# Kernel tuning notes

Hardware: AMD Instinct MI355X
Metric: run time of the kernel (lower is better)

Reference implementation:

```python
import jax, jax.numpy as jnp
import numpy as np

T, B, I, H, O = 512, 64, 512, 1024, 512
STDV = 1.0 / np.sqrt(H)


def setup_inputs() -> dict:
    key = jax.random.key(0)
    ks = jax.random.split(key, 12)
    u = lambda k, shape: jax.random.uniform(k, shape, jnp.float32, -STDV, STDV)
    return {
        "input": jax.random.normal(ks[0], (T, B, I), jnp.float32),
        "state": jnp.zeros((B, H), jnp.float32),
        "W_zh": u(ks[1], (H, H)), "W_zx": u(ks[2], (I, H)), "b_z": u(ks[3], (H,)),
        "W_rh": u(ks[4], (H, H)), "W_rx": u(ks[5], (I, H)), "b_r": u(ks[6], (H,)),
        "W_hh": u(ks[7], (H, H)), "W_hx": u(ks[8], (I, H)), "b_h": u(ks[9], (H,)),
        "W_out": u(ks[10], (O, H)), "b_out": u(ks[11], (O,)),
    }


def reference(input, state, W_zh, W_zx, b_z, W_rh, W_rx, b_r, W_hh, W_hx, b_h, W_out, b_out):
    # input: [T, B, I]; state: [B, H]
    def step(h, x):
        z = jax.nn.sigmoid(h @ W_zh + x @ W_zx + b_z)
        r = jax.nn.sigmoid(h @ W_rh + x @ W_rx + b_r)
        ht = jnp.tanh((h * r) @ W_hh + x @ W_hx + b_h)
        h = (1.0 - z) * h + z * ht
        y = h @ W_out.T + b_out  # Linear(hidim -> outdim)
        return h, y

    h_final, Y = jax.lax.scan(step, state, input)  # Y: [T, B, O]
    # torch.cat(Y, dim=0) -> [T*B, O]
    return Y.reshape(T * B, O), h_final
```

## Files before the change

### kernel.cpp

```cpp
#include <hip/hip_runtime.h>
#include <cstdint>


#define TT 512
#define BB 64
#define II 512
#define HH 1024
#define OO 512
#define NTHR 512

typedef float4 f4;
__device__ __forceinline__ f4 ld4(const float* p){ return *reinterpret_cast<const f4*>(p); }
__device__ __forceinline__ int swz(int k){ return k ^ (((k >> 4) & 7) << 2); }

__device__ __forceinline__ void ldc16(const float* p, f4* d){
  asm volatile(
    "global_load_dwordx4 %0,  %16, off sc0 sc1\n\t"
    "global_load_dwordx4 %1,  %16, off offset:256 sc0 sc1\n\t"
    "global_load_dwordx4 %2,  %16, off offset:512 sc0 sc1\n\t"
    "global_load_dwordx4 %3,  %16, off offset:768 sc0 sc1\n\t"
    "global_load_dwordx4 %4,  %16, off offset:1024 sc0 sc1\n\t"
    "global_load_dwordx4 %5,  %16, off offset:1280 sc0 sc1\n\t"
    "global_load_dwordx4 %6,  %16, off offset:1536 sc0 sc1\n\t"
    "global_load_dwordx4 %7,  %16, off offset:1792 sc0 sc1\n\t"
    "global_load_dwordx4 %8,  %16, off offset:2048 sc0 sc1\n\t"
    "global_load_dwordx4 %9,  %16, off offset:2304 sc0 sc1\n\t"
    "global_load_dwordx4 %10, %16, off offset:2560 sc0 sc1\n\t"
    "global_load_dwordx4 %11, %16, off offset:2816 sc0 sc1\n\t"
    "global_load_dwordx4 %12, %16, off offset:3072 sc0 sc1\n\t"
    "global_load_dwordx4 %13, %16, off offset:3328 sc0 sc1\n\t"
    "global_load_dwordx4 %14, %16, off offset:3584 sc0 sc1\n\t"
    "s_waitcnt vmcnt(1)\n\t"
    "global_load_dwordx4 %15, %16, off offset:3840 sc0 sc1\n\t"
    "s_waitcnt vmcnt(0)"
    : "=&v"(d[0]),"=&v"(d[1]),"=&v"(d[2]),"=&v"(d[3]),
      "=&v"(d[4]),"=&v"(d[5]),"=&v"(d[6]),"=&v"(d[7]),
      "=&v"(d[8]),"=&v"(d[9]),"=&v"(d[10]),"=&v"(d[11]),
      "=&v"(d[12]),"=&v"(d[13]),"=&v"(d[14]),"=&v"(d[15])
    : "v"(p) : "memory");
}
__device__ __forceinline__ float ldc1(const float* p){
  float v;
  asm volatile("global_load_dword %0, %1, off sc0 sc1\n\ts_waitcnt vmcnt(0)"
               : "=v"(v) : "v"(p) : "memory");
  return v;
}
__device__ __forceinline__ void stc1(float* p, float v){
  asm volatile("global_store_dword %0, %1, off sc0 sc1" :: "v"(p), "v"(v) : "memory");
}

__global__ void k_transpose_x(const float* __restrict__ x, float* __restrict__ xT){
  size_t total = (size_t)TT * II * BB;
  for (size_t n = (size_t)blockIdx.x * blockDim.x + threadIdx.x; n < total;
       n += (size_t)gridDim.x * blockDim.x){
    size_t t = n / ((size_t)II * BB);
    size_t rem = n % ((size_t)II * BB);
    size_t i = rem / BB, b = rem % BB;
    xT[n] = x[(t * BB + b) * II + i];
  }
}

__global__ void k_transpose_wx(const float* __restrict__ W, float* __restrict__ WT){
  size_t n = (size_t)blockIdx.x * blockDim.x + threadIdx.x;
  if (n >= (size_t)II * HH) return;
  size_t j = n / II, k = n % II;
  WT[n] = W[k * HH + j];
}

__global__ void k_transpose_h0(const float* __restrict__ st, float* __restrict__ h0){
  size_t n = (size_t)blockIdx.x * blockDim.x + threadIdx.x;
  if (n >= (size_t)HH * BB) return;
  size_t j = n / BB, b = n % BB;
  h0[n] = st[b * HH + j];
}

__global__ void k_init_bars(unsigned* bars){
  if (threadIdx.x < 512) bars[threadIdx.x] = 0;
}

__device__ __forceinline__ void g_arrive(unsigned* bars, int g, int jt, unsigned ep){
  asm volatile("s_waitcnt vmcnt(0)" ::: "memory");
  unsigned* leaf = bars + (g * 9 + (jt & 7)) * 16;
  unsigned old = __hip_atomic_fetch_add(leaf, 1u, __ATOMIC_RELAXED, __HIP_MEMORY_SCOPE_AGENT);
  if (old + 1u == ep * 16u)
    __hip_atomic_fetch_add(bars + (g * 9 + 8) * 16, 1u, __ATOMIC_RELAXED, __HIP_MEMORY_SCOPE_AGENT);
}
__device__ __forceinline__ void g_wait(unsigned* bars, int g, unsigned ep){
  unsigned* root = bars + (g * 9 + 8) * 16;
  while (__hip_atomic_load(root, __ATOMIC_RELAXED, __HIP_MEMORY_SCOPE_AGENT) < ep * 8u)
    __builtin_amdgcn_s_sleep(1);
}

#define WREDUCE(v) { v += __shfl_xor(v, 8); v += __shfl_xor(v, 16); v += __shfl_xor(v, 32); }

__global__ __launch_bounds__(NTHR, 2) void k_gru(
    const float* __restrict__ xT,
    const float* __restrict__ WxTr, const float* __restrict__ WxTz, const float* __restrict__ WxTh,
    float* __restrict__ h, float* __restrict__ s,
    const float* __restrict__ W_zh, const float* __restrict__ b_z,
    const float* __restrict__ W_rh, const float* __restrict__ b_r,
    const float* __restrict__ W_hh, const float* __restrict__ b_h,
    const float* __restrict__ W_out, const float* __restrict__ b_out,
    float* __restrict__ out, unsigned* __restrict__ bars)
{
  __shared__ float sW[3 * 8 * 1024];
  __shared__ float red[8 * 528];
  __shared__ float xpre[3][256];
  __shared__ float sZ[256];
  __shared__ float sBias[32];

  const int tid = threadIdx.x;
  const int bid = blockIdx.x;
  const int jt = bid & 127, bhalf = bid >> 7;
  const int j0 = jt * 8, o0 = jt * 4, bbase = bhalf * 32;

  #pragma unroll
  for (int kk2 = 0; kk2 < 2; ++kk2){
    const int k = tid * 2 + kk2;
    f4 vr  = ld4(W_rh + (size_t)k * HH + j0);
    f4 vr2 = ld4(W_rh + (size_t)k * HH + j0 + 4);
    f4 vz  = ld4(W_zh + (size_t)k * HH + j0);
    f4 vz2 = ld4(W_zh + (size_t)k * HH + j0 + 4);
    f4 vh  = ld4(W_hh + (size_t)k * HH + j0);
    f4 vh2 = ld4(W_hh + (size_t)k * HH + j0 + 4);
    const int kx = swz(k);
    float ar[8] = {vr.x,vr.y,vr.z,vr.w,vr2.x,vr2.y,vr2.z,vr2.w};
    float az[8] = {vz.x,vz.y,vz.z,vz.w,vz2.x,vz2.y,vz2.z,vz2.w};
    float ah[8] = {vh.x,vh.y,vh.z,vh.w,vh2.x,vh2.y,vh2.z,vh2.w};
    #pragma unroll
    for (int c = 0; c < 8; ++c){
      sW[0*8192 + c*1024 + kx] = ar[c];
      sW[1*8192 + c*1024 + kx] = az[c];
      sW[2*8192 + c*1024 + kx] = ah[c];
    }
  }
  if (tid < 8){
    sBias[tid]      = b_r[j0 + tid];
    sBias[8 + tid]  = b_z[j0 + tid];
    sBias[16 + tid] = b_h[j0 + tid];
    if (tid < 4) sBias[24 + tid] = b_out[o0 + tid];
  }

  const int bg = tid & 7, b0 = bbase + bg * 4;
  const int ksec = tid >> 3;
  const int wv = tid >> 6;
  const bool wr0 = ((tid & 56) == 0);
  const int kh0 = ksec * 16;
  const int kx0 = ksec * 8;
  __syncthreads();

  for (int t = -1; t < TT; ++t){
    f4 st4[16];
    if (t >= 0){
      float aR[8][4] = {};
      ldc16(h + kh0 * BB + b0, st4);
      #pragma unroll
      for (int i4 = 0; i4 < 4; ++i4){
        const int kxc = swz(kh0 + i4*4);
        #pragma unroll
        for (int c = 0; c < 8; ++c){
          f4 wf = *reinterpret_cast<const f4*>(&sW[0*8192 + c*1024 + kxc]);
          float wvv[4] = {wf.x, wf.y, wf.z, wf.w};
          #pragma unroll
          for (int kk = 0; kk < 4; ++kk){
            const f4 hv = st4[i4*4+kk];
            aR[c][0] = fmaf(wvv[kk], hv.x, aR[c][0]);
            aR[c][1] = fmaf(wvv[kk], hv.y, aR[c][1]);
            aR[c][2] = fmaf(wvv[kk], hv.z, aR[c][2]);
            aR[c][3] = fmaf(wvv[kk], hv.w, aR[c][3]);
          }
        }
      }
      #pragma unroll
      for (int c = 0; c < 8; ++c)
        #pragma unroll
        for (int bb = 0; bb < 4; ++bb) WREDUCE(aR[c][bb]);
      if (wr0)
        #pragma unroll
        for (int c = 0; c < 8; ++c)
          #pragma unroll
          for (int bb = 0; bb < 4; ++bb)
            red[wv*528 + c*32 + bg*4 + bb] = aR[c][bb];
      __syncthreads();
      if (tid < 256){
        float sum = 0.f;
        #pragma unroll
        for (int w = 0; w < 8; ++w) sum += red[w*528 + tid];
        const int c = tid >> 5, bl = tid & 31;
        const float v = sum + xpre[0][tid] + sBias[c];
        const float rr = 1.f / (1.f + expf(-v));
        const int jg = j0 + c, bgl = bbase + bl;
        stc1(&s[jg*BB + bgl], rr * ldc1(&h[jg*BB + bgl]));
      }
      __syncthreads();
      if (tid == 0) g_arrive(bars, bhalf, jt, 2*t + 1);

      float aZ[8][4] = {};
      float aY[4][4] = {};
      #pragma unroll
      for (int i4 = 0; i4 < 4; ++i4){
        const int kc = kh0 + i4*4;
        const int kxc = swz(kc);
        #pragma unroll
        for (int c = 0; c < 8; ++c){
          f4 wf = *reinterpret_cast<const f4*>(&sW[1*8192 + c*1024 + kxc]);
          float wvv[4] = {wf.x, wf.y, wf.z, wf.w};
          #pragma unroll
          for (int kk = 0; kk < 4; ++kk){
            const f4 hv = st4[i4*4+kk];
            aZ[c][0] = fmaf(wvv[kk], hv.x, aZ[c][0]);
            aZ[c][1] = fmaf(wvv[kk], hv.y, aZ[c][1]);
            aZ[c][2] = fmaf(wvv[kk], hv.z, aZ[c][2]);
            aZ[c][3] = fmaf(wvv[kk], hv.w, aZ[c][3]);
          }
        }
        #pragma unroll
        for (int oc = 0; oc < 4; ++oc){
          f4 wo = ld4(W_out + (size_t)(o0 + oc) * HH + kc);
          float wvv[4] = {wo.x, wo.y, wo.z, wo.w};
          #pragma unroll
          for (int kk = 0; kk < 4; ++kk){
            const f4 hv = st4[i4*4+kk];
            aY[oc][0] = fmaf(wvv[kk], hv.x, aY[oc][0]);
            aY[oc][1] = fmaf(wvv[kk], hv.y, aY[oc][1]);
            aY[oc][2] = fmaf(wvv[kk], hv.z, aY[oc][2]);
            aY[oc][3] = fmaf(wvv[kk], hv.w, aY[oc][3]);
          }
        }
      }
      #pragma unroll
      for (int c = 0; c < 8; ++c)
        #pragma unroll
        for (int bb = 0; bb < 4; ++bb) WREDUCE(aZ[c][bb]);
      #pragma unroll
      for (int oc = 0; oc < 4; ++oc)
        #pragma unroll
        for (int bb = 0; bb < 4; ++bb) WREDUCE(aY[oc][bb]);
      if (wr0){
        #pragma unroll
        for (int c = 0; c < 8; ++c)
          #pragma unroll
          for (int bb = 0; bb < 4; ++bb)
            red[wv*528 + c*32 + bg*4 + bb] = aZ[c][bb];
        #pragma unroll
        for (int oc = 0; oc < 4; ++oc)
          #pragma unroll
          for (int bb = 0; bb < 4; ++bb)
            red[wv*528 + 256 + oc*32 + bg*4 + bb] = aY[oc][bb];
      }
      __syncthreads();
      if (tid < 256){
        float sum = 0.f;
        #pragma unroll
        for (int w = 0; w < 8; ++w) sum += red[w*528 + tid];
        const int c = tid >> 5;
        sZ[tid] = 1.f / (1.f + expf(-(sum + xpre[1][tid] + sBias[8 + c])));
      } else if (tid < 384){
        const int idx = tid - 256;
        float sum = 0.f;
        #pragma unroll
        for (int w = 0; w < 8; ++w) sum += red[w*528 + tid];
        const int oc = idx >> 5, bl = idx & 31;
        if (t > 0)
          out[((size_t)(t-1)*BB + bbase + bl)*OO + o0 + oc] = sum + sBias[24 + oc];
      }
      if (tid == 0) g_wait(bars, bhalf, 2*t + 1);
      __syncthreads();

      float aH[8][4] = {};
      f4 sv16[16];
      ldc16(s + kh0 * BB + b0, sv16);
      #pragma unroll
      for (int i4 = 0; i4 < 4; ++i4){
        const int kxc = swz(kh0 + i4*4);
        #pragma unroll
        for (int c = 0; c < 8; ++c){
          f4 wf = *reinterpret_cast<const f4*>(&sW[2*8192 + c*1024 + kxc]);
          float wvv[4] = {wf.x, wf.y, wf.z, wf.w};
          #pragma unroll
          for (int kk = 0; kk < 4; ++kk){
            const f4 sv = sv16[i4*4+kk];
            aH[c][0] = fmaf(wvv[kk], sv.x, aH[c][0]);
            aH[c][1] = fmaf(wvv[kk], sv.y, aH[c][1]);
            aH[c][2] = fmaf(wvv[kk], sv.z, aH[c][2]);
            aH[c][3] = fmaf(wvv[kk], sv.w, aH[c][3]);
          }
        }
      }
      #pragma unroll
      for (int c = 0; c < 8; ++c)
        #pragma unroll
        for (int bb = 0; bb < 4; ++bb) WREDUCE(aH[c][bb]);
      if (wr0)
        #pragma unroll
        for (int c = 0; c < 8; ++c)
          #pragma unroll
          for (int bb = 0; bb < 4; ++bb)
            red[wv*528 + c*32 + bg*4 + bb] = aH[c][bb];
      __syncthreads();
      if (tid < 256){
        float sum = 0.f;
        #pragma unroll
        for (int w = 0; w < 8; ++w) sum += red[w*528 + tid];
        const int c = tid >> 5, bl = tid & 31;
        const int jg = j0 + c, bgl = bbase + bl;
        const float ht = tanhf(sum + xpre[2][tid] + sBias[16 + c]);
        const float z = sZ[tid];
        const float hold = ldc1(&h[jg*BB + bgl]);
        const float hnew = fmaf(z, ht - hold, hold);
        stc1(&h[jg*BB + bgl], hnew);
        if (t == TT - 1) out[(size_t)TT*BB*OO + (size_t)bgl*HH + jg] = hnew;
      }
      __syncthreads();
      if (tid == 0) g_arrive(bars, bhalf, jt, 2*t + 2);
    }

    if (t + 1 < TT){
      const int tc = t + 1;
      float aXr[8][4] = {}, aXz[8][4] = {}, aXh[8][4] = {};
      const float* xb = xT + (size_t)tc * II * BB + kx0 * BB + b0;
      #pragma unroll
      for (int i4 = 0; i4 < 2; ++i4){
        f4 xv4[4];
        #pragma unroll
        for (int kk = 0; kk < 4; ++kk) xv4[kk] = ld4(xb + (i4*4+kk) * BB);
        #pragma unroll
        for (int c = 0; c < 8; ++c){
          f4 wr_ = ld4(WxTr + (size_t)(j0 + c) * II + kx0 + i4*4);
          f4 wz_ = ld4(WxTz + (size_t)(j0 + c) * II + kx0 + i4*4);
          f4 wh_ = ld4(WxTh + (size_t)(j0 + c) * II + kx0 + i4*4);
          float wrv[4] = {wr_.x, wr_.y, wr_.z, wr_.w};
          float wzv[4] = {wz_.x, wz_.y, wz_.z, wz_.w};
          float whv[4] = {wh_.x, wh_.y, wh_.z, wh_.w};
          #pragma unroll
          for (int kk = 0; kk < 4; ++kk){
            const f4 xv = xv4[kk];
            aXr[c][0] = fmaf(wrv[kk], xv.x, aXr[c][0]);
            aXr[c][1] = fmaf(wrv[kk], xv.y, aXr[c][1]);
            aXr[c][2] = fmaf(wrv[kk], xv.z, aXr[c][2]);
            aXr[c][3] = fmaf(wrv[kk], xv.w, aXr[c][3]);
            aXz[c][0] = fmaf(wzv[kk], xv.x, aXz[c][0]);
            aXz[c][1] = fmaf(wzv[kk], xv.y, aXz[c][1]);
            aXz[c][2] = fmaf(wzv[kk], xv.z, aXz[c][2]);
            aXz[c][3] = fmaf(wzv[kk], xv.w, aXz[c][3]);
            aXh[c][0] = fmaf(whv[kk], xv.x, aXh[c][0]);
            aXh[c][1] = fmaf(whv[kk], xv.y, aXh[c][1]);
            aXh[c][2] = fmaf(whv[kk], xv.z, aXh[c][2]);
            aXh[c][3] = fmaf(whv[kk], xv.w, aXh[c][3]);
          }
        }
      }
      #pragma unroll
      for (int c = 0; c < 8; ++c)
        #pragma unroll
        for (int bb = 0; bb < 4; ++bb){ WREDUCE(aXr[c][bb]); WREDUCE(aXz[c][bb]); WREDUCE(aXh[c][bb]); }
      if (wr0)
        #pragma unroll
        for (int c = 0; c < 8; ++c)
          #pragma unroll
          for (int bb = 0; bb < 4; ++bb){
            red[wv*528 + c*32 + bg*4 + bb]       = aXr[c][bb];
            red[wv*528 + 256 + c*32 + bg*4 + bb] = aXz[c][bb];
          }
      __syncthreads();
      {
        float sum = 0.f;
        #pragma unroll
        for (int w = 0; w < 8; ++w) sum += red[w*528 + tid];
        if (tid < 256) xpre[0][tid] = sum;
        else           xpre[1][tid - 256] = sum;
      }
      __syncthreads();
      if (wr0)
        #pragma unroll
        for (int c = 0; c < 8; ++c)
          #pragma unroll
          for (int bb = 0; bb < 4; ++bb)
            red[wv*528 + c*32 + bg*4 + bb] = aXh[c][bb];
      __syncthreads();
      if (tid < 256){
        float sum = 0.f;
        #pragma unroll
        for (int w = 0; w < 8; ++w) sum += red[w*528 + tid];
        xpre[2][tid] = sum;
      }
      __syncthreads();
    }

    if (t >= 0){
      if (tid == 0) g_wait(bars, bhalf, 2*t + 2);
      __syncthreads();
    }
  }

  {
    float aY[4][4] = {};
    f4 hv16[16];
    ldc16(h + kh0 * BB + b0, hv16);
    #pragma unroll
    for (int i4 = 0; i4 < 4; ++i4){
      const int kc = kh0 + i4*4;
      #pragma unroll
      for (int oc = 0; oc < 4; ++oc){
        f4 wo = ld4(W_out + (size_t)(o0 + oc) * HH + kc);
        float wvv[4] = {wo.x, wo.y, wo.z, wo.w};
        #pragma unroll
        for (int kk = 0; kk < 4; ++kk){
          const f4 hv = hv16[i4*4+kk];
          aY[oc][0] = fmaf(wvv[kk], hv.x, aY[oc][0]);
          aY[oc][1] = fmaf(wvv[kk], hv.y, aY[oc][1]);
          aY[oc][2] = fmaf(wvv[kk], hv.z, aY[oc][2]);
          aY[oc][3] = fmaf(wvv[kk], hv.w, aY[oc][3]);
        }
      }
    }
    #pragma unroll
    for (int oc = 0; oc < 4; ++oc)
      #pragma unroll
      for (int bb = 0; bb < 4; ++bb) WREDUCE(aY[oc][bb]);
    if (wr0)
      #pragma unroll
      for (int oc = 0; oc < 4; ++oc)
        #pragma unroll
        for (int bb = 0; bb < 4; ++bb)
          red[wv*528 + oc*32 + bg*4 + bb] = aY[oc][bb];
    __syncthreads();
    if (tid < 128){
      float sum = 0.f;
      #pragma unroll
      for (int w = 0; w < 8; ++w) sum += red[w*528 + tid];
      const int oc = tid >> 5, bl = tid & 31;
      out[((size_t)(TT-1)*BB + bbase + bl)*OO + o0 + oc] = sum + sBias[24 + oc];
    }
  }
}

extern "C" void kernel_launch(void* const* d_in, const int* in_sizes, int n_in,
                              void* d_out, int out_size, void* d_ws, size_t ws_size,
                              hipStream_t stream) {
  const float* x     = (const float*)d_in[0];
  const float* st    = (const float*)d_in[1];
  const float* W_zh  = (const float*)d_in[2];
  const float* W_zx  = (const float*)d_in[3];
  const float* b_z   = (const float*)d_in[4];
  const float* W_rh  = (const float*)d_in[5];
  const float* W_rx  = (const float*)d_in[6];
  const float* b_r   = (const float*)d_in[7];
  const float* W_hh  = (const float*)d_in[8];
  const float* W_hx  = (const float*)d_in[9];
  const float* b_h   = (const float*)d_in[10];
  const float* W_out = (const float*)d_in[11];
  const float* b_out = (const float*)d_in[12];
  float* out = (float*)d_out;
  float* ws  = (float*)d_ws;

  const size_t xT_sz = (size_t)TT * II * BB;
  const size_t wx_sz = (size_t)II * HH;
  const size_t h_sz  = (size_t)HH * BB;
  const size_t need  = (xT_sz + 3*wx_sz + 2*h_sz) * sizeof(float) + 512*sizeof(unsigned);
  if (ws_size < need) return;

  float* xT   = ws;
  float* WxTr = xT + xT_sz;
  float* WxTz = WxTr + wx_sz;
  float* WxTh = WxTz + wx_sz;
  float* h    = WxTh + wx_sz;
  float* s    = h + h_sz;
  unsigned* bars = (unsigned*)(s + h_sz);

  k_transpose_x <<<8192, 256, 0, stream>>>(x, xT);
  k_transpose_wx<<<2048, 256, 0, stream>>>(W_rx, WxTr);
  k_transpose_wx<<<2048, 256, 0, stream>>>(W_zx, WxTz);
  k_transpose_wx<<<2048, 256, 0, stream>>>(W_hx, WxTh);
  k_transpose_h0<<< 256, 256, 0, stream>>>(st, h);
  k_init_bars   <<<   1, 512, 0, stream>>>(bars);

  k_gru<<<256, NTHR, 0, stream>>>(xT, WxTr, WxTz, WxTh, h, s,
                                  W_zh, b_z, W_rh, b_r, W_hh, b_h,
                                  W_out, b_out, out, bars);
}
```

Measured before the change: 12.98 ms.

## Read input directly in native layout, drop transpose kernel and LDS reduction

Removes the separate transpose of the full input sequence and has the GRU kernel read x in its original [T,B,I] layout. Each thread now handles one batch row and a contiguous 32-element k slice, so the x-projection partial sums are reduced entirely with intra-wavefront shuffles rather than through shared memory with three block barriers. This saves a large global read/write pass and several syncs per timestep. The cost is more weight-load traffic per thread, since each thread loads 32 k values of weights for a single batch element and gets less reuse than before.

```diff
diff --git a/kernel.cpp b/kernel.cpp
--- a/kernel.cpp
+++ b/kernel.cpp
@@ -49,17 +49,6 @@
   asm volatile("global_store_dword %0, %1, off sc0 sc1" :: "v"(p), "v"(v) : "memory");
 }
 
-__global__ void k_transpose_x(const float* __restrict__ x, float* __restrict__ xT){
-  size_t total = (size_t)TT * II * BB;
-  for (size_t n = (size_t)blockIdx.x * blockDim.x + threadIdx.x; n < total;
-       n += (size_t)gridDim.x * blockDim.x){
-    size_t t = n / ((size_t)II * BB);
-    size_t rem = n % ((size_t)II * BB);
-    size_t i = rem / BB, b = rem % BB;
-    xT[n] = x[(t * BB + b) * II + i];
-  }
-}
-
 __global__ void k_transpose_wx(const float* __restrict__ W, float* __restrict__ WT){
   size_t n = (size_t)blockIdx.x * blockDim.x + threadIdx.x;
   if (n >= (size_t)II * HH) return;
@@ -94,7 +83,7 @@
 #define WREDUCE(v) { v += __shfl_xor(v, 8); v += __shfl_xor(v, 16); v += __shfl_xor(v, 32); }
 
 __global__ __launch_bounds__(NTHR, 2) void k_gru(
-    const float* __restrict__ xT,
+    const float* __restrict__ x,
     const float* __restrict__ WxTr, const float* __restrict__ WxTz, const float* __restrict__ WxTh,
     float* __restrict__ h, float* __restrict__ s,
     const float* __restrict__ W_zh, const float* __restrict__ b_z,
@@ -146,7 +135,10 @@
   const int wv = tid >> 6;
   const bool wr0 = ((tid & 56) == 0);
   const int kh0 = ksec * 16;
-  const int kx0 = ksec * 8;
+
+  const int bC  = bbase + (tid >> 4);
+  const int ksC = tid & 15;
+  const int k0C = ksC * 32;
   __syncthreads();
 
   for (int t = -1; t < TT; ++t){
@@ -317,72 +309,48 @@
 
     if (t + 1 < TT){
       const int tc = t + 1;
-      float aXr[8][4] = {}, aXz[8][4] = {}, aXh[8][4] = {};
-      const float* xb = xT + (size_t)tc * II * BB + kx0 * BB + b0;
-      #pragma unroll
-      for (int i4 = 0; i4 < 2; ++i4){
-        f4 xv4[4];
-        #pragma unroll
-        for (int kk = 0; kk < 4; ++kk) xv4[kk] = ld4(xb + (i4*4+kk) * BB);
+      const float* xb = x + ((size_t)tc * BB + bC) * II + k0C;
+      float aX[3][8];
+      #pragma unroll
+      for (int g = 0; g < 3; ++g)
+        #pragma unroll
+        for (int c = 0; c < 8; ++c) aX[g][c] = 0.f;
+      #pragma unroll
+      for (int i4 = 0; i4 < 8; ++i4){
+        f4 xv = ld4(xb + i4*4);
+        float xvv[4] = {xv.x, xv.y, xv.z, xv.w};
         #pragma unroll
         for (int c = 0; c < 8; ++c){
-          f4 wr_ = ld4(WxTr + (size_t)(j0 + c) * II + kx0 + i4*4);
-          f4 wz_ = ld4(WxTz + (size_t)(j0 + c) * II + kx0 + i4*4);
-          f4 wh_ = ld4(WxTh + (size_t)(j0 + c) * II + kx0 + i4*4);
+          f4 wr_ = ld4(WxTr + (size_t)(j0 + c) * II + k0C + i4*4);
+          f4 wz_ = ld4(WxTz + (size_t)(j0 + c) * II + k0C + i4*4);
+          f4 wh_ = ld4(WxTh + (size_t)(j0 + c) * II + k0C + i4*4);
           float wrv[4] = {wr_.x, wr_.y, wr_.z, wr_.w};
           float wzv[4] = {wz_.x, wz_.y, wz_.z, wz_.w};
           float whv[4] = {wh_.x, wh_.y, wh_.z, wh_.w};
           #pragma unroll
           for (int kk = 0; kk < 4; ++kk){
-            const f4 xv = xv4[kk];
-            aXr[c][0] = fmaf(wrv[kk], xv.x, aXr[c][0]);
-            aXr[c][1] = fmaf(wrv[kk], xv.y, aXr[c][1]);
-            aXr[c][2] = fmaf(wrv[kk], xv.z, aXr[c][2]);
-            aXr[c][3] = fmaf(wrv[kk], xv.w, aXr[c][3]);
-            aXz[c][0] = fmaf(wzv[kk], xv.x, aXz[c][0]);
-            aXz[c][1] = fmaf(wzv[kk], xv.y, aXz[c][1]);
-            aXz[c][2] = fmaf(wzv[kk], xv.z, aXz[c][2]);
-            aXz[c][3] = fmaf(wzv[kk], xv.w, aXz[c][3]);
-            aXh[c][0] = fmaf(whv[kk], xv.x, aXh[c][0]);
-            aXh[c][1] = fmaf(whv[kk], xv.y, aXh[c][1]);
-            aXh[c][2] = fmaf(whv[kk], xv.z, aXh[c][2]);
-            aXh[c][3] = fmaf(whv[kk], xv.w, aXh[c][3]);
+            aX[0][c] = fmaf(wrv[kk], xvv[kk], aX[0][c]);
+            aX[1][c] = fmaf(wzv[kk], xvv[kk], aX[1][c]);
+            aX[2][c] = fmaf(whv[kk], xvv[kk], aX[2][c]);
           }
         }
       }
       #pragma unroll
-      for (int c = 0; c < 8; ++c)
-        #pragma unroll
-        for (int bb = 0; bb < 4; ++bb){ WREDUCE(aXr[c][bb]); WREDUCE(aXz[c][bb]); WREDUCE(aXh[c][bb]); }
-      if (wr0)
-        #pragma unroll
-        for (int c = 0; c < 8; ++c)
-          #pragma unroll
-          for (int bb = 0; bb < 4; ++bb){
-            red[wv*528 + c*32 + bg*4 + bb]       = aXr[c][bb];
-            red[wv*528 + 256 + c*32 + bg*4 + bb] = aXz[c][bb];
-          }
-      __syncthreads();
-      {
-        float sum = 0.f;
-        #pragma unroll
-        for (int w = 0; w < 8; ++w) sum += red[w*528 + tid];
-        if (tid < 256) xpre[0][tid] = sum;
-        else           xpre[1][tid - 256] = sum;
-      }
-      __syncthreads();
-      if (wr0)
-        #pragma unroll
-        for (int c = 0; c < 8; ++c)
-          #pragma unroll
-          for (int bb = 0; bb < 4; ++bb)
-            red[wv*528 + c*32 + bg*4 + bb] = aXh[c][bb];
-      __syncthreads();
-      if (tid < 256){
-        float sum = 0.f;
-        #pragma unroll
-        for (int w = 0; w < 8; ++w) sum += red[w*528 + tid];
-        xpre[2][tid] = sum;
+      for (int g = 0; g < 3; ++g)
+        #pragma unroll
+        for (int c = 0; c < 8; ++c){
+          aX[g][c] += __shfl_xor(aX[g][c], 1);
+          aX[g][c] += __shfl_xor(aX[g][c], 2);
+          aX[g][c] += __shfl_xor(aX[g][c], 4);
+          aX[g][c] += __shfl_xor(aX[g][c], 8);
+        }
+      if (ksC == 0){
+        const int bl = bC - bbase;
+        #pragma unroll
+        for (int g = 0; g < 3; ++g)
+          #pragma unroll
+          for (int c = 0; c < 8; ++c)
+            xpre[g][c*32 + bl] = aX[g][c];
       }
       __syncthreads();
     }
@@ -454,28 +422,25 @@
   float* out = (float*)d_out;
   float* ws  = (float*)d_ws;
 
-  const size_t xT_sz = (size_t)TT * II * BB;
   const size_t wx_sz = (size_t)II * HH;
   const size_t h_sz  = (size_t)HH * BB;
-  const size_t need  = (xT_sz + 3*wx_sz + 2*h_sz) * sizeof(float) + 512*sizeof(unsigned);
+  const size_t need  = (3*wx_sz + 2*h_sz) * sizeof(float) + 512*sizeof(unsigned);
   if (ws_size < need) return;
 
-  float* xT   = ws;
-  float* WxTr = xT + xT_sz;
+  float* WxTr = ws;
   float* WxTz = WxTr + wx_sz;
   float* WxTh = WxTz + wx_sz;
   float* h    = WxTh + wx_sz;
   float* s    = h + h_sz;
   unsigned* bars = (unsigned*)(s + h_sz);
 
-  k_transpose_x <<<8192, 256, 0, stream>>>(x, xT);
   k_transpose_wx<<<2048, 256, 0, stream>>>(W_rx, WxTr);
   k_transpose_wx<<<2048, 256, 0, stream>>>(W_zx, WxTz);
   k_transpose_wx<<<2048, 256, 0, stream>>>(W_hx, WxTh);
   k_transpose_h0<<< 256, 256, 0, stream>>>(st, h);
   k_init_bars   <<<   1, 512, 0, stream>>>(bars);
 
-  k_gru<<<256, NTHR, 0, stream>>>(xT, WxTr, WxTz, WxTh, h, s,
+  k_gru<<<256, NTHR, 0, stream>>>(x, WxTr, WxTz, WxTh, h, s,
                                   W_zh, b_z, W_rh, b_r, W_hh, b_h,
                                   W_out, b_out, out, bars);
 }
```

Measured after the change: 33.03 ms. 2.54x slower.
